# Kernel optimization log

Measured on AMD Instinct MI355X. Metric: run time of the kernel, lower is better.

The kernel has to match this reference:

```python
import jax, jax.numpy as jnp
import numpy as np

KS = 3      # kernel_size
PAD = 1     # zero padding
N = KS * KS # sampling points per pixel
PI = 3.1415926


def conv2d(x, w, b=None, stride=1, padding=0):
    out = jax.lax.conv_general_dilated(
        x, w, (stride, stride), [(padding, padding), (padding, padding)],
        dimension_numbers=('NCHW', 'OIHW', 'NCHW'))
    if b is not None:
        out = out + b[None, :, None, None]
    return out


def setup_inputs() -> dict:
    key = jax.random.key(0)
    ks = jax.random.split(key, 8)
    B, C, OUTC, H, W = 4, 64, 64, 128, 128
    x = jax.random.normal(ks[0], (B, C, H, W), jnp.float32)
    w_b = jax.random.normal(ks[1], (OUTC, C, 3, 3), jnp.float32) * 0.05
    b_b = jax.random.normal(ks[2], (OUTC,), jnp.float32) * 0.05
    w_p = jax.random.normal(ks[3], (3, C, 3, 3), jnp.float32) * 0.05
    b_p = jax.random.normal(ks[4], (3,), jnp.float32) * 0.05
    w_m = jax.random.normal(ks[5], (N, C, 3, 3), jnp.float32) * 0.05
    b_m = jax.random.normal(ks[6], (N,), jnp.float32) * 0.05
    w_c = jax.random.normal(ks[7], (OUTC, C, 3, 3), jnp.float32) * 0.05
    return {"x": x, "w_b": w_b, "b_b": b_b, "w_p": w_p, "b_p": b_p,
            "w_m": w_m, "b_m": b_m, "w_c": w_c}


def reference(x, w_b, b_b, w_p, b_p, w_m, b_m, w_c):
    B, C, H, W = x.shape
    # bias branch: plain 3x3 conv, stride 1, pad 1
    bias = conv2d(x, w_b, b_b, stride=1, padding=1)
    # offset branch: conv -> sin -> (dropout eval = id) -> sigmoid
    off = jax.nn.sigmoid(jnp.sin(conv2d(x, w_p, b_p, stride=1, padding=1)))  # [B,3,H,W]
    l = off[:, 0] * 48.5 + 1.5          # [B,H,W] rect length
    wd = off[:, 1] * 48.5 + 1.5         # [B,H,W] rect width
    theta = off[:, 2] * PI              # [B,H,W] rotation angle
    # modulation mask
    m = jax.nn.sigmoid(conv2d(x, w_m, b_m, stride=1, padding=1))  # [B,9,H,W]

    # zero-pad input for sampling
    xp = jnp.pad(x, ((0, 0), (0, 0), (PAD, PAD), (PAD, PAD)))
    Hp, Wp = H + 2 * PAD, W + 2 * PAD

    # kernel grid offsets (ij meshgrid, x flattened first)
    rng = jnp.arange(-(KS - 1) // 2, (KS - 1) // 2 + 1, dtype=jnp.float32)
    pn_x = jnp.repeat(rng, KS)  # [N]  (-1,-1,-1,0,0,0,1,1,1)
    pn_y = jnp.tile(rng, KS)    # [N]  (-1,0,1,-1,0,1,-1,0,1)
    p0_x = jnp.arange(1, H + 1, dtype=jnp.float32)[:, None, None]  # [H,1,1]
    p0_y = jnp.arange(1, W + 1, dtype=jnp.float32)[None, :, None]  # [1,W,1]

    # sampling positions p = p0 + offset/3 * p_n, per point: [B,H,W,N]
    px = p0_x + (l[..., None] / 3.0) * pn_x
    py = p0_y + (wd[..., None] / 3.0) * pn_y
    ct = jnp.cos(theta)[..., None]  # [B,H,W,1]
    st = jnp.sin(theta)[..., None]
    pxx = px * ct - py * st
    pyy = px * st + py * ct

    # integer corners (non-diff, matches .detach().floor())
    fx = jnp.floor(jax.lax.stop_gradient(pxx))
    fy = jnp.floor(jax.lax.stop_gradient(pyy))
    qlt_x = jnp.clip(fx, 0, Hp - 1).astype(jnp.int32)
    qlt_y = jnp.clip(fy, 0, Wp - 1).astype(jnp.int32)
    qrb_x = jnp.clip(fx + 1, 0, Hp - 1).astype(jnp.int32)
    qrb_y = jnp.clip(fy + 1, 0, Wp - 1).astype(jnp.int32)

    # clamp continuous positions
    pcx = jnp.clip(pxx, 0, Hp - 1)
    pcy = jnp.clip(pyy, 0, Wp - 1)

    # bilinear weights
    g_lt = (1 + (qlt_x - pcx)) * (1 + (qlt_y - pcy))
    g_rb = (1 - (qrb_x - pcx)) * (1 - (qrb_y - pcy))
    g_lb = (1 + (qlt_x - pcx)) * (1 - (qrb_y - pcy))
    g_rt = (1 - (qrb_x - pcx)) * (1 + (qlt_y - pcy))

    # gather four corners: [B,C,H,W,N]
    def _gather_one(xp_b, qx_b, qy_b):
        return xp_b[:, qx_b, qy_b]  # [C,H,W,N]
    gather = jax.vmap(_gather_one)
    x_lt = gather(xp, qlt_x, qlt_y)
    x_rb = gather(xp, qrb_x, qrb_y)
    x_lb = gather(xp, qlt_x, qrb_y)
    x_rt = gather(xp, qrb_x, qlt_y)

    x_off = (g_lt[:, None] * x_lt + g_rb[:, None] * x_rb +
             g_lb[:, None] * x_lb + g_rt[:, None] * x_rt)  # [B,C,H,W,N]
    # modulation: [B,9,H,W] -> [B,1,H,W,9]
    x_off = x_off * jnp.transpose(m, (0, 2, 3, 1))[:, None]

    # rearrange [B,C,H,W,ks*ks] -> [B,C,H*ks,W*ks]
    x_off = x_off.reshape(B, C, H, W, KS, KS)
    x_off = jnp.transpose(x_off, (0, 1, 2, 4, 3, 5)).reshape(B, C, H * KS, W * KS)

    out = conv2d(x_off, w_c, None, stride=KS, padding=0) + bias
    return out
```

## Files before the change

kernel.cpp:

```cpp
#include <hip/hip_runtime.h>
#include <hip/hip_bf16.h>
#include <math.h>

#define BB 4
#define CC 64
#define OC 64
#define HH 128
#define WW 128
#define HP 130
#define WP 130
#define KTOT 1152
#define NKK 36
#define NKC 18
#define PIXT 32

#define XP_OFF 0
#define WR8_OFF 4326400
#define WPM8_OFF (4326400 + 36864)

typedef __attribute__((ext_vector_type(8))) short bf16x8;
typedef __attribute__((ext_vector_type(4))) short bf16x4;
typedef __attribute__((ext_vector_type(4))) float f32x4;

__device__ __forceinline__ unsigned short f2bf(float v) {
    union { float f; unsigned int u; } x; x.f = v;
    unsigned int r = x.u + 0x7FFF + ((x.u >> 16) & 1);
    return (unsigned short)(r >> 16);
}

__device__ __forceinline__ unsigned short f2bfh(float v) {
    __hip_bfloat16 h = __float2bfloat16(v);
    return *reinterpret_cast<unsigned short*>(&h);
}

__device__ __forceinline__ float fexp_(float x) {
    return __builtin_amdgcn_exp2f(x * 1.44269504089f);
}
__device__ __forceinline__ float fsig_(float z) {
    return __builtin_amdgcn_rcpf(1.f + fexp_(-z));
}
__device__ __forceinline__ float fsin_(float x) {
    float r = x * 0.15915494309f;
    r = __builtin_amdgcn_fractf(r);
    return __builtin_amdgcn_sinf(r);
}
__device__ __forceinline__ float fcos_(float x) {
    float r = x * 0.15915494309f;
    r = __builtin_amdgcn_fractf(r);
    return __builtin_amdgcn_cosf(r);
}

#define NB_TR 1024
#define NB_BZ 516
#define NB_WR 288
#define NB_WPM 36

__global__ __launch_bounds__(256) void k_prep(
    const float* __restrict__ x,
    const float* __restrict__ w_b, const float* __restrict__ w_c,
    const float* __restrict__ w_p, const float* __restrict__ w_m,
    float* __restrict__ xp, unsigned short* __restrict__ wr8,
    unsigned short* __restrict__ wpm8)
{
    int bi = blockIdx.x;
    int tid = threadIdx.x;
    if (bi < NB_TR) {
        __shared__ float t[64][65];
        int b = bi >> 8;
        int h = (bi >> 1) & 127;
        int w0 = (bi & 1) * 64;
        int lane6 = tid & 63;
        for (int cc = tid >> 6; cc < 64; cc += 4)
            t[cc][lane6] = x[((b * 64 + cc) * 128 + h) * 128 + w0 + lane6];
        __syncthreads();
        for (int wsub = tid >> 6; wsub < 64; wsub += 4)
            xp[((size_t)(b * HP + h + 1) * WP + (w0 + wsub + 1)) * 64 + lane6] = t[lane6][wsub];
        return;
    }
    bi -= NB_TR;
    if (bi < NB_BZ) {
        int idx = bi * 256 + tid;
        int c = idx & 63;
        int tt = idx >> 6;
        int b = tt / 516;
        int j = tt % 516;
        int hp, wp;
        if (j < 130)      { hp = 0;       wp = j; }
        else if (j < 260) { hp = 129;     wp = j - 130; }
        else if (j < 388) { hp = j - 259; wp = 0; }
        else              { hp = j - 387; wp = 129; }
        xp[((size_t)(b * HP + hp) * WP + wp) * 64 + c] = 0.f;
        return;
    }
    bi -= NB_BZ;
    if (bi < NB_WR) {
        int idx = bi * 256 + tid;
        int j    = idx & 7;
        int lane = (idx >> 3) & 63;
        int ot   = (idx >> 9) & 3;
        int kk   = idx >> 11;
        int o  = ot * 16 + (lane & 15);
        int k  = kk * 32 + (lane >> 4) * 8 + j;
        int slot = k >> 6;
        int c    = k & 63;
        float v;
        if (slot < 9) v = w_b[((o * CC + c) * 3 + slot / 3) * 3 + slot % 3];
        else { int n = slot - 9; v = w_c[((o * CC + c) * 3 + n / 3) * 3 + n % 3]; }
        wr8[idx] = f2bf(v);
        return;
    }
    bi -= NB_WR;
    {
        int idx = bi * 256 + tid;
        if (idx >= NKC * 64 * 8) return;
        int j    = idx & 7;
        int lane = (idx >> 3) & 63;
        int kk   = idx >> 9;
        int ch = lane & 15;
        int k  = kk * 32 + (lane >> 4) * 8 + j;
        int tap = k >> 6;
        int c   = k & 63;
        float v = 0.f;
        if (ch < 3)       v = w_p[((ch * CC + c) * 3 + tap / 3) * 3 + tap % 3];
        else if (ch < 12) v = w_m[(((ch - 3) * CC + c) * 3 + tap / 3) * 3 + tap % 3];
        wpm8[idx] = f2bf(v);
    }
}

__global__ __launch_bounds__(512, 4) void k_main(
    const float* __restrict__ xp, const unsigned short* __restrict__ wr8,
    const unsigned short* __restrict__ wpm8,
    const float* __restrict__ w_p,
    const float* __restrict__ b_p, const float* __restrict__ b_m,
    const float* __restrict__ b_b, float* __restrict__ out)
{
    __shared__ unsigned short U8[2 * 18432];
    __shared__ float wth[16][9][4];

    int tid = threadIdx.x;
    int lane = tid & 63;
    int g = tid >> 6;
    int p_sub = lane >> 4;
    int cq = lane & 15;
    int c0 = cq * 4;

    int bid = blockIdx.x;
    int swz = (bid & 7) * 256 + (bid >> 3);
    int pixBase = swz * PIXT;

    for (int i = tid; i < 576; i += 512) {
        int cqi = i / 36;
        int rest = i % 36;
        int tap = rest >> 2;
        int e = rest & 3;
        int c = cqi * 4 + e;
        wth[cqi][tap][e] = w_p[((2 * CC + c) * 3 + tap / 3) * 3 + tap % 3];
    }
    __syncthreads();

    int p_local = g * 4 + p_sub;
    int ph = p_local >> 4;
    int p16 = p_local & 15;
    int pix = pixBase + p_local;
    int b = pix >> 14;
    int h = (pix >> 7) & 127;
    int w = pix & 127;
    const float* xb = xp + (size_t)b * HP * WP * 64;

    float th = 0.f;
#pragma unroll
    for (int tap = 0; tap < 9; ++tap) {
        int ti = tap / 3, tj = tap % 3;
        float4 xv = *(const float4*)&xb[((h + ti) * WP + (w + tj)) * 64 + c0];
        float4 wt = *(const float4*)&wth[cq][tap][0];
        th += xv.x * wt.x + xv.y * wt.y + xv.z * wt.z + xv.w * wt.w;
        int k = tap * 64 + c0;
        int kqt = k >> 3;
        int blk = kqt * 16 + (p16 ^ (kqt & 15));
        bf16x4 pk;
        pk[0] = (short)f2bfh(xv.x); pk[1] = (short)f2bfh(xv.y);
        pk[2] = (short)f2bfh(xv.z); pk[3] = (short)f2bfh(xv.w);
        *(bf16x4*)&U8[ph * 18432 + blk * 8 + (k & 7)] = pk;
    }
    th += __shfl_xor(th, 1);
    th += __shfl_xor(th, 2);
    th += __shfl_xor(th, 4);
    th += __shfl_xor(th, 8);

    int kq = lane >> 4;
    f32x4 ca = {0.f, 0.f, 0.f, 0.f}, cb = {0.f, 0.f, 0.f, 0.f};
    {
        int colp = lane & 3;
        int pabs = g * 4 + colp;
        int phc = g >> 2;
        int p16c = pabs & 15;
        const bf16x8* av = (const bf16x8*)wpm8;
#pragma unroll
        for (int kk = 0; kk < NKC; ++kk) {
            bf16x8 a = av[kk * 64 + lane];
            int kqt = kk * 4 + kq;
            int blk = kqt * 16 + (p16c ^ (kqt & 15));
            bf16x8 bf = *(const bf16x8*)&U8[phc * 18432 + blk * 8];
            if (kk & 1) cb = __builtin_amdgcn_mfma_f32_16x16x32_bf16(a, bf, cb, 0, 0, 0);
            else        ca = __builtin_amdgcn_mfma_f32_16x16x32_bf16(a, bf, ca, 0, 0, 0);
        }
        ca[0] += cb[0]; ca[1] += cb[1]; ca[2] += cb[2]; ca[3] += cb[3];
    }

    int base16 = p_sub << 4;
    int chc = (cq < 9) ? (3 + cq) : 3;
    int srcL = ((chc >> 2) << 4) + p_sub;
    float m0 = __shfl(ca[0], srcL);
    float m1 = __shfl(ca[1], srcL);
    float m2 = __shfl(ca[2], srcL);
    float m3 = __shfl(ca[3], srcL);
    int jj = chc & 3;
    float cm = (jj == 0) ? m0 : (jj == 1) ? m1 : (jj == 2) ? m2 : m3;
    float c0v = __shfl(ca[0], p_sub);
    float c1v = __shfl(ca[1], p_sub);

    float bp0 = b_p[0], bp1 = b_p[1], bp2 = b_p[2];
    float hval = 0.f;
    if (cq == 9)       hval = fsig_(fsin_(c0v + bp0)) * 48.5f + 1.5f;
    else if (cq == 10) hval = fsig_(fsin_(c1v + bp1)) * 48.5f + 1.5f;
    else if (cq == 11) hval = fcos_(fsig_(fsin_(th + bp2)) * 3.1415926f);
    else if (cq == 12) hval = fsin_(fsig_(fsin_(th + bp2)) * 3.1415926f);
    float l  = __shfl(hval, base16 + 9);
    float wd = __shfl(hval, base16 + 10);
    float ct = __shfl(hval, base16 + 11);
    float st = __shfl(hval, base16 + 12);

    unsigned int qpack; float glt, grb, glb, grt;
    {
        int n = (cq < 9) ? cq : 8;
        float mm = fsig_(cm + b_m[n]);
        float pnx = (float)(n / 3 - 1);
        float pny = (float)(n % 3 - 1);
        float px = (float)(h + 1) + (l * (1.f / 3.f)) * pnx;
        float py = (float)(w + 1) + (wd * (1.f / 3.f)) * pny;
        float pxx = px * ct - py * st;
        float pyy = px * st + py * ct;
        float fx = floorf(pxx);
        float fy = floorf(pyy);
        int qltx = min(max((int)fx, 0), HP - 1);
        int qlty = min(max((int)fy, 0), WP - 1);
        int qrbx = min(max((int)fx + 1, 0), HP - 1);
        int qrby = min(max((int)fy + 1, 0), WP - 1);
        float pcx = fminf(fmaxf(pxx, 0.f), (float)(HP - 1));
        float pcy = fminf(fmaxf(pyy, 0.f), (float)(WP - 1));
        float dltx = 1.f + ((float)qltx - pcx);
        float drbx = 1.f - ((float)qrbx - pcx);
        float dlty = 1.f + ((float)qlty - pcy);
        float drby = 1.f - ((float)qrby - pcy);
        glt = dltx * dlty * mm;
        grb = drbx * drby * mm;
        glb = dltx * drby * mm;
        grt = drbx * dlty * mm;
        qpack = (unsigned)qltx | ((unsigned)qlty << 8) |
                ((unsigned)qrbx << 16) | ((unsigned)qrby << 24);
    }

    unsigned int qn[9];
    float wlt[9], wrb[9], wlb[9], wrt[9];
#pragma unroll
    for (int n = 0; n < 9; ++n) {
        qn[n]  = __shfl(qpack, base16 + n);
        wlt[n] = __shfl(glt, base16 + n);
        wrb[n] = __shfl(grb, base16 + n);
        wlb[n] = __shfl(glb, base16 + n);
        wrt[n] = __shfl(grt, base16 + n);
    }

#pragma unroll
    for (int n = 0; n < 9; ++n) {
        unsigned int q = qn[n];
        int qltx = q & 255, qlty = (q >> 8) & 255;
        int qrbx = (q >> 16) & 255, qrby = (q >> 24) & 255;
        float4 xlt = *(const float4*)&xb[(qltx * WP + qlty) * 64 + c0];
        float4 xrb = *(const float4*)&xb[(qrbx * WP + qrby) * 64 + c0];
        float4 xlb = *(const float4*)&xb[(qltx * WP + qrby) * 64 + c0];
        float4 xrt = *(const float4*)&xb[(qrbx * WP + qlty) * 64 + c0];
        float g_lt = wlt[n], g_rb = wrb[n], g_lb = wlb[n], g_rt = wrt[n];
        float v0 = g_lt * xlt.x + g_rb * xrb.x + g_lb * xlb.x + g_rt * xrt.x;
        float v1 = g_lt * xlt.y + g_rb * xrb.y + g_lb * xlb.y + g_rt * xrt.y;
        float v2 = g_lt * xlt.z + g_rb * xrb.z + g_lb * xlb.z + g_rt * xrt.z;
        float v3 = g_lt * xlt.w + g_rb * xrb.w + g_lb * xlb.w + g_rt * xrt.w;
        int k = (9 + n) * 64 + c0;
        int kqt = k >> 3;
        int blk = kqt * 16 + (p16 ^ (kqt & 15));
        bf16x4 pk;
        pk[0] = (short)f2bfh(v0); pk[1] = (short)f2bfh(v1);
        pk[2] = (short)f2bfh(v2); pk[3] = (short)f2bfh(v3);
        *(bf16x4*)&U8[ph * 18432 + blk * 8 + (k & 7)] = pk;
    }
    __syncthreads();

    int ot = g & 3;
    int ph2 = g >> 2;
    int pn = lane & 15;
    f32x4 a0 = {0.f, 0.f, 0.f, 0.f}, a1 = {0.f, 0.f, 0.f, 0.f};
    const bf16x8* wv = (const bf16x8*)wr8;
#pragma unroll
    for (int kk = 0; kk < NKK; ++kk) {
        bf16x8 a = wv[(kk * 4 + ot) * 64 + lane];
        int kqt = kk * 4 + kq;
        int blk = kqt * 16 + (pn ^ (kqt & 15));
        bf16x8 bf = *(const bf16x8*)&U8[ph2 * 18432 + blk * 8];
        if (kk & 1) a1 = __builtin_amdgcn_mfma_f32_16x16x32_bf16(a, bf, a1, 0, 0, 0);
        else        a0 = __builtin_amdgcn_mfma_f32_16x16x32_bf16(a, bf, a0, 0, 0, 0);
    }

    int pix2 = pixBase + ph2 * 16 + pn;
    int bb2 = pix2 >> 14;
    int hw = pix2 & 16383;
#pragma unroll
    for (int r2 = 0; r2 < 4; ++r2) {
        int o = ot * 16 + kq * 4 + r2;
        out[((size_t)(bb2 * 64 + o)) * 16384 + hw] = a0[r2] + a1[r2] + b_b[o];
    }
}

extern "C" void kernel_launch(void* const* d_in, const int* in_sizes, int n_in,
                              void* d_out, int out_size, void* d_ws, size_t ws_size,
                              hipStream_t stream) {
    const float* x   = (const float*)d_in[0];
    const float* w_b = (const float*)d_in[1];
    const float* b_b = (const float*)d_in[2];
    const float* w_p = (const float*)d_in[3];
    const float* b_p = (const float*)d_in[4];
    const float* w_m = (const float*)d_in[5];
    const float* b_m = (const float*)d_in[6];
    const float* w_c = (const float*)d_in[7];
    float* out = (float*)d_out;

    float* ws = (float*)d_ws;
    float* xp = ws + XP_OFF;
    unsigned short* wr8  = (unsigned short*)(ws + WR8_OFF);
    unsigned short* wpm8 = (unsigned short*)(ws + WPM8_OFF);

    k_prep<<<NB_TR + NB_BZ + NB_WR + NB_WPM, 256, 0, stream>>>(
        x, w_b, w_c, w_p, w_m, xp, wr8, wpm8);
    k_main<<<(BB * HH * WW) / PIXT, 512, 0, stream>>>(
        xp, wr8, wpm8, w_p, b_p, b_m, b_b, out);
}
```

Before: 70.13 us.

## Double pixel tile per block to reuse weight fragments across two MFMA tiles

Each block now processes 64 pixels instead of 32. It runs the sampling and packing stage twice into a doubled LDS buffer, then in the main GEMM loads each weight fragment once and feeds two MFMAs, one per 16-pixel half. This halves global weight-fragment traffic per pixel and halves the block count. The cost is twice the LDS per block (about 147KB), lower occupancy (launch bounds 2), and serialized gather work per block.

```diff
diff --git a/kernel.cpp b/kernel.cpp
--- a/kernel.cpp
+++ b/kernel.cpp
@@ -12,7 +12,7 @@
 #define KTOT 1152
 #define NKK 36
 #define NKC 18
-#define PIXT 32
+#define PIXT 64
 
 #define XP_OFF 0
 #define WR8_OFF 4326400
@@ -127,14 +127,14 @@
     }
 }
 
-__global__ __launch_bounds__(512, 4) void k_main(
+__global__ __launch_bounds__(512, 2) void k_main(
     const float* __restrict__ xp, const unsigned short* __restrict__ wr8,
     const unsigned short* __restrict__ wpm8,
     const float* __restrict__ w_p,
     const float* __restrict__ b_p, const float* __restrict__ b_m,
     const float* __restrict__ b_b, float* __restrict__ out)
 {
-    __shared__ unsigned short U8[2 * 18432];
+    __shared__ unsigned short U8[4 * 18432];
     __shared__ float wth[16][9][4];
 
     int tid = threadIdx.x;
@@ -143,9 +143,10 @@
     int p_sub = lane >> 4;
     int cq = lane & 15;
     int c0 = cq * 4;
+    int kq = lane >> 4;
 
     int bid = blockIdx.x;
-    int swz = (bid & 7) * 256 + (bid >> 3);
+    int swz = (bid & 7) * 128 + (bid >> 3);
     int pixBase = swz * PIXT;
 
     for (int i = tid; i < 576; i += 512) {
@@ -158,165 +159,179 @@
     }
     __syncthreads();
 
-    int p_local = g * 4 + p_sub;
-    int ph = p_local >> 4;
-    int p16 = p_local & 15;
-    int pix = pixBase + p_local;
-    int b = pix >> 14;
-    int h = (pix >> 7) & 127;
-    int w = pix & 127;
-    const float* xb = xp + (size_t)b * HP * WP * 64;
-
-    float th = 0.f;
-#pragma unroll
-    for (int tap = 0; tap < 9; ++tap) {
-        int ti = tap / 3, tj = tap % 3;
-        float4 xv = *(const float4*)&xb[((h + ti) * WP + (w + tj)) * 64 + c0];
-        float4 wt = *(const float4*)&wth[cq][tap][0];
-        th += xv.x * wt.x + xv.y * wt.y + xv.z * wt.z + xv.w * wt.w;
-        int k = tap * 64 + c0;
-        int kqt = k >> 3;
-        int blk = kqt * 16 + (p16 ^ (kqt & 15));
-        bf16x4 pk;
-        pk[0] = (short)f2bfh(xv.x); pk[1] = (short)f2bfh(xv.y);
-        pk[2] = (short)f2bfh(xv.z); pk[3] = (short)f2bfh(xv.w);
-        *(bf16x4*)&U8[ph * 18432 + blk * 8 + (k & 7)] = pk;
-    }
-    th += __shfl_xor(th, 1);
-    th += __shfl_xor(th, 2);
-    th += __shfl_xor(th, 4);
-    th += __shfl_xor(th, 8);
-
-    int kq = lane >> 4;
-    f32x4 ca = {0.f, 0.f, 0.f, 0.f}, cb = {0.f, 0.f, 0.f, 0.f};
-    {
-        int colp = lane & 3;
-        int pabs = g * 4 + colp;
-        int phc = g >> 2;
-        int p16c = pabs & 15;
-        const bf16x8* av = (const bf16x8*)wpm8;
-#pragma unroll
-        for (int kk = 0; kk < NKC; ++kk) {
-            bf16x8 a = av[kk * 64 + lane];
-            int kqt = kk * 4 + kq;
-            int blk = kqt * 16 + (p16c ^ (kqt & 15));
-            bf16x8 bf = *(const bf16x8*)&U8[phc * 18432 + blk * 8];
-            if (kk & 1) cb = __builtin_amdgcn_mfma_f32_16x16x32_bf16(a, bf, cb, 0, 0, 0);
-            else        ca = __builtin_amdgcn_mfma_f32_16x16x32_bf16(a, bf, ca, 0, 0, 0);
-        }
-        ca[0] += cb[0]; ca[1] += cb[1]; ca[2] += cb[2]; ca[3] += cb[3];
-    }
-
-    int base16 = p_sub << 4;
-    int chc = (cq < 9) ? (3 + cq) : 3;
-    int srcL = ((chc >> 2) << 4) + p_sub;
-    float m0 = __shfl(ca[0], srcL);
-    float m1 = __shfl(ca[1], srcL);
-    float m2 = __shfl(ca[2], srcL);
-    float m3 = __shfl(ca[3], srcL);
-    int jj = chc & 3;
-    float cm = (jj == 0) ? m0 : (jj == 1) ? m1 : (jj == 2) ? m2 : m3;
-    float c0v = __shfl(ca[0], p_sub);
-    float c1v = __shfl(ca[1], p_sub);
-
-    float bp0 = b_p[0], bp1 = b_p[1], bp2 = b_p[2];
-    float hval = 0.f;
-    if (cq == 9)       hval = fsig_(fsin_(c0v + bp0)) * 48.5f + 1.5f;
-    else if (cq == 10) hval = fsig_(fsin_(c1v + bp1)) * 48.5f + 1.5f;
-    else if (cq == 11) hval = fcos_(fsig_(fsin_(th + bp2)) * 3.1415926f);
-    else if (cq == 12) hval = fsin_(fsig_(fsin_(th + bp2)) * 3.1415926f);
-    float l  = __shfl(hval, base16 + 9);
-    float wd = __shfl(hval, base16 + 10);
-    float ct = __shfl(hval, base16 + 11);
-    float st = __shfl(hval, base16 + 12);
-
-    unsigned int qpack; float glt, grb, glb, grt;
-    {
-        int n = (cq < 9) ? cq : 8;
-        float mm = fsig_(cm + b_m[n]);
-        float pnx = (float)(n / 3 - 1);
-        float pny = (float)(n % 3 - 1);
-        float px = (float)(h + 1) + (l * (1.f / 3.f)) * pnx;
-        float py = (float)(w + 1) + (wd * (1.f / 3.f)) * pny;
-        float pxx = px * ct - py * st;
-        float pyy = px * st + py * ct;
-        float fx = floorf(pxx);
-        float fy = floorf(pyy);
-        int qltx = min(max((int)fx, 0), HP - 1);
-        int qlty = min(max((int)fy, 0), WP - 1);
-        int qrbx = min(max((int)fx + 1, 0), HP - 1);
-        int qrby = min(max((int)fy + 1, 0), WP - 1);
-        float pcx = fminf(fmaxf(pxx, 0.f), (float)(HP - 1));
-        float pcy = fminf(fmaxf(pyy, 0.f), (float)(WP - 1));
-        float dltx = 1.f + ((float)qltx - pcx);
-        float drbx = 1.f - ((float)qrbx - pcx);
-        float dlty = 1.f + ((float)qlty - pcy);
-        float drby = 1.f - ((float)qrby - pcy);
-        glt = dltx * dlty * mm;
-        grb = drbx * drby * mm;
-        glb = dltx * drby * mm;
-        grt = drbx * dlty * mm;
-        qpack = (unsigned)qltx | ((unsigned)qlty << 8) |
-                ((unsigned)qrbx << 16) | ((unsigned)qrby << 24);
-    }
-
-    unsigned int qn[9];
-    float wlt[9], wrb[9], wlb[9], wrt[9];
-#pragma unroll
-    for (int n = 0; n < 9; ++n) {
-        qn[n]  = __shfl(qpack, base16 + n);
-        wlt[n] = __shfl(glt, base16 + n);
-        wrb[n] = __shfl(grb, base16 + n);
-        wlb[n] = __shfl(glb, base16 + n);
-        wrt[n] = __shfl(grt, base16 + n);
-    }
-
-#pragma unroll
-    for (int n = 0; n < 9; ++n) {
-        unsigned int q = qn[n];
-        int qltx = q & 255, qlty = (q >> 8) & 255;
-        int qrbx = (q >> 16) & 255, qrby = (q >> 24) & 255;
-        float4 xlt = *(const float4*)&xb[(qltx * WP + qlty) * 64 + c0];
-        float4 xrb = *(const float4*)&xb[(qrbx * WP + qrby) * 64 + c0];
-        float4 xlb = *(const float4*)&xb[(qltx * WP + qrby) * 64 + c0];
-        float4 xrt = *(const float4*)&xb[(qrbx * WP + qlty) * 64 + c0];
-        float g_lt = wlt[n], g_rb = wrb[n], g_lb = wlb[n], g_rt = wrt[n];
-        float v0 = g_lt * xlt.x + g_rb * xrb.x + g_lb * xlb.x + g_rt * xrt.x;
-        float v1 = g_lt * xlt.y + g_rb * xrb.y + g_lb * xlb.y + g_rt * xrt.y;
-        float v2 = g_lt * xlt.z + g_rb * xrb.z + g_lb * xlb.z + g_rt * xrt.z;
-        float v3 = g_lt * xlt.w + g_rb * xrb.w + g_lb * xlb.w + g_rt * xrt.w;
-        int k = (9 + n) * 64 + c0;
-        int kqt = k >> 3;
-        int blk = kqt * 16 + (p16 ^ (kqt & 15));
-        bf16x4 pk;
-        pk[0] = (short)f2bfh(v0); pk[1] = (short)f2bfh(v1);
-        pk[2] = (short)f2bfh(v2); pk[3] = (short)f2bfh(v3);
-        *(bf16x4*)&U8[ph * 18432 + blk * 8 + (k & 7)] = pk;
+    for (int pp = 0; pp < 2; ++pp) {
+        int p_local = g * 4 + p_sub + pp * 32;
+        int ph = p_local >> 4;
+        int p16 = p_local & 15;
+        int pix = pixBase + p_local;
+        int b = pix >> 14;
+        int h = (pix >> 7) & 127;
+        int w = pix & 127;
+        const float* xb = xp + (size_t)b * HP * WP * 64;
+
+        float th = 0.f;
+#pragma unroll
+        for (int tap = 0; tap < 9; ++tap) {
+            int ti = tap / 3, tj = tap % 3;
+            float4 xv = *(const float4*)&xb[((h + ti) * WP + (w + tj)) * 64 + c0];
+            float4 wt = *(const float4*)&wth[cq][tap][0];
+            th += xv.x * wt.x + xv.y * wt.y + xv.z * wt.z + xv.w * wt.w;
+            int k = tap * 64 + c0;
+            int kqt = k >> 3;
+            int blk = kqt * 16 + (p16 ^ (kqt & 15));
+            bf16x4 pk;
+            pk[0] = (short)f2bfh(xv.x); pk[1] = (short)f2bfh(xv.y);
+            pk[2] = (short)f2bfh(xv.z); pk[3] = (short)f2bfh(xv.w);
+            *(bf16x4*)&U8[ph * 18432 + blk * 8 + (k & 7)] = pk;
+        }
+        th += __shfl_xor(th, 1);
+        th += __shfl_xor(th, 2);
+        th += __shfl_xor(th, 4);
+        th += __shfl_xor(th, 8);
+
+        f32x4 ca = {0.f, 0.f, 0.f, 0.f}, cb = {0.f, 0.f, 0.f, 0.f};
+        {
+            int colp = lane & 3;
+            int pabs = g * 4 + colp;
+            int phc = (g >> 2) + 2 * pp;
+            int p16c = pabs & 15;
+            const bf16x8* av = (const bf16x8*)wpm8;
+#pragma unroll
+            for (int kk = 0; kk < NKC; ++kk) {
+                bf16x8 a = av[kk * 64 + lane];
+                int kqt = kk * 4 + kq;
+                int blk = kqt * 16 + (p16c ^ (kqt & 15));
+                bf16x8 bf = *(const bf16x8*)&U8[phc * 18432 + blk * 8];
+                if (kk & 1) cb = __builtin_amdgcn_mfma_f32_16x16x32_bf16(a, bf, cb, 0, 0, 0);
+                else        ca = __builtin_amdgcn_mfma_f32_16x16x32_bf16(a, bf, ca, 0, 0, 0);
+            }
+            ca[0] += cb[0]; ca[1] += cb[1]; ca[2] += cb[2]; ca[3] += cb[3];
+        }
+
+        int base16 = p_sub << 4;
+        int chc = (cq < 9) ? (3 + cq) : 3;
+        int srcL = ((chc >> 2) << 4) + p_sub;
+        float m0 = __shfl(ca[0], srcL);
+        float m1 = __shfl(ca[1], srcL);
+        float m2 = __shfl(ca[2], srcL);
+        float m3 = __shfl(ca[3], srcL);
+        int jj = chc & 3;
+        float cm = (jj == 0) ? m0 : (jj == 1) ? m1 : (jj == 2) ? m2 : m3;
+        float c0v = __shfl(ca[0], p_sub);
+        float c1v = __shfl(ca[1], p_sub);
+
+        float bp0 = b_p[0], bp1 = b_p[1], bp2 = b_p[2];
+        float hval = 0.f;
+        if (cq == 9)       hval = fsig_(fsin_(c0v + bp0)) * 48.5f + 1.5f;
+        else if (cq == 10) hval = fsig_(fsin_(c1v + bp1)) * 48.5f + 1.5f;
+        else if (cq == 11) hval = fcos_(fsig_(fsin_(th + bp2)) * 3.1415926f);
+        else if (cq == 12) hval = fsin_(fsig_(fsin_(th + bp2)) * 3.1415926f);
+        float l  = __shfl(hval, base16 + 9);
+        float wd = __shfl(hval, base16 + 10);
+        float ct = __shfl(hval, base16 + 11);
+        float st = __shfl(hval, base16 + 12);
+
+        unsigned int qpack; float glt, grb, glb, grt;
+        {
+            int n = (cq < 9) ? cq : 8;
+            float mm = fsig_(cm + b_m[n]);
+            float pnx = (float)(n / 3 - 1);
+            float pny = (float)(n % 3 - 1);
+            float px = (float)(h + 1) + (l * (1.f / 3.f)) * pnx;
+            float py = (float)(w + 1) + (wd * (1.f / 3.f)) * pny;
+            float pxx = px * ct - py * st;
+            float pyy = px * st + py * ct;
+            float fx = floorf(pxx);
+            float fy = floorf(pyy);
+            int qltx = min(max((int)fx, 0), HP - 1);
+            int qlty = min(max((int)fy, 0), WP - 1);
+            int qrbx = min(max((int)fx + 1, 0), HP - 1);
+            int qrby = min(max((int)fy + 1, 0), WP - 1);
+            float pcx = fminf(fmaxf(pxx, 0.f), (float)(HP - 1));
+            float pcy = fminf(fmaxf(pyy, 0.f), (float)(WP - 1));
+            float dltx = 1.f + ((float)qltx - pcx);
+            float drbx = 1.f - ((float)qrbx - pcx);
+            float dlty = 1.f + ((float)qlty - pcy);
+            float drby = 1.f - ((float)qrby - pcy);
+            glt = dltx * dlty * mm;
+            grb = drbx * drby * mm;
+            glb = dltx * drby * mm;
+            grt = drbx * dlty * mm;
+            qpack = (unsigned)qltx | ((unsigned)qlty << 8) |
+                    ((unsigned)qrbx << 16) | ((unsigned)qrby << 24);
+        }
+
+        unsigned int qn[9];
+        float wlt[9], wrb[9], wlb[9], wrt[9];
+#pragma unroll
+        for (int n = 0; n < 9; ++n) {
+            qn[n]  = __shfl(qpack, base16 + n);
+            wlt[n] = __shfl(glt, base16 + n);
+            wrb[n] = __shfl(grb, base16 + n);
+            wlb[n] = __shfl(glb, base16 + n);
+            wrt[n] = __shfl(grt, base16 + n);
+        }
+
+#pragma unroll
+        for (int n = 0; n < 9; ++n) {
+            unsigned int q = qn[n];
+            int qltx = q & 255, qlty = (q >> 8) & 255;
+            int qrbx = (q >> 16) & 255, qrby = (q >> 24) & 255;
+            float4 xlt = *(const float4*)&xb[(qltx * WP + qlty) * 64 + c0];
+            float4 xrb = *(const float4*)&xb[(qrbx * WP + qrby) * 64 + c0];
+            float4 xlb = *(const float4*)&xb[(qltx * WP + qrby) * 64 + c0];
+            float4 xrt = *(const float4*)&xb[(qrbx * WP + qlty) * 64 + c0];
+            float g_lt = wlt[n], g_rb = wrb[n], g_lb = wlb[n], g_rt = wrt[n];
+            float v0 = g_lt * xlt.x + g_rb * xrb.x + g_lb * xlb.x + g_rt * xrt.x;
+            float v1 = g_lt * xlt.y + g_rb * xrb.y + g_lb * xlb.y + g_rt * xrt.y;
+            float v2 = g_lt * xlt.z + g_rb * xrb.z + g_lb * xlb.z + g_rt * xrt.z;
+            float v3 = g_lt * xlt.w + g_rb * xrb.w + g_lb * xlb.w + g_rt * xrt.w;
+            int k = (9 + n) * 64 + c0;
+            int kqt = k >> 3;
+            int blk = kqt * 16 + (p16 ^ (kqt & 15));
+            bf16x4 pk;
+            pk[0] = (short)f2bfh(v0); pk[1] = (short)f2bfh(v1);
+            pk[2] = (short)f2bfh(v2); pk[3] = (short)f2bfh(v3);
+            *(bf16x4*)&U8[ph * 18432 + blk * 8 + (k & 7)] = pk;
+        }
     }
     __syncthreads();
 
     int ot = g & 3;
-    int ph2 = g >> 2;
+    int hA = g >> 2;
     int pn = lane & 15;
-    f32x4 a0 = {0.f, 0.f, 0.f, 0.f}, a1 = {0.f, 0.f, 0.f, 0.f};
+    f32x4 accA = {0.f, 0.f, 0.f, 0.f}, accB = {0.f, 0.f, 0.f, 0.f};
     const bf16x8* wv = (const bf16x8*)wr8;
 #pragma unroll
     for (int kk = 0; kk < NKK; ++kk) {
         bf16x8 a = wv[(kk * 4 + ot) * 64 + lane];
         int kqt = kk * 4 + kq;
         int blk = kqt * 16 + (pn ^ (kqt & 15));
-        bf16x8 bf = *(const bf16x8*)&U8[ph2 * 18432 + blk * 8];
-        if (kk & 1) a1 = __builtin_amdgcn_mfma_f32_16x16x32_bf16(a, bf, a1, 0, 0, 0);
-        else        a0 = __builtin_amdgcn_mfma_f32_16x16x32_bf16(a, bf, a0, 0, 0, 0);
-    }
-
-    int pix2 = pixBase + ph2 * 16 + pn;
-    int bb2 = pix2 >> 14;
-    int hw = pix2 & 16383;
-#pragma unroll
-    for (int r2 = 0; r2 < 4; ++r2) {
-        int o = ot * 16 + kq * 4 + r2;
-        out[((size_t)(bb2 * 64 + o)) * 16384 + hw] = a0[r2] + a1[r2] + b_b[o];
+        bf16x8 bA = *(const bf16x8*)&U8[hA * 18432 + blk * 8];
+        bf16x8 bB = *(const bf16x8*)&U8[(hA + 2) * 18432 + blk * 8];
+        accA = __builtin_amdgcn_mfma_f32_16x16x32_bf16(a, bA, accA, 0, 0, 0);
+        accB = __builtin_amdgcn_mfma_f32_16x16x32_bf16(a, bB, accB, 0, 0, 0);
+    }
+
+    {
+        int pix2 = pixBase + hA * 16 + pn;
+        int bb2 = pix2 >> 14;
+        int hw = pix2 & 16383;
+#pragma unroll
+        for (int r2 = 0; r2 < 4; ++r2) {
+            int o = ot * 16 + kq * 4 + r2;
+            out[((size_t)(bb2 * 64 + o)) * 16384 + hw] = accA[r2] + b_b[o];
+        }
+    }
+    {
+        int pix2 = pixBase + (hA + 2) * 16 + pn;
+        int bb2 = pix2 >> 14;
+        int hw = pix2 & 16383;
+#pragma unroll
+        for (int r2 = 0; r2 < 4; ++r2) {
+            int o = ot * 16 + kq * 4 + r2;
+            out[((size_t)(bb2 * 64 + o)) * 16384 + hw] = accB[r2] + b_b[o];
+        }
     }
 }
 
```

After: 79.03 us. +12.7%, slower.

## Halve LDS staging by splitting main GEMM into two K-phases, stage sampling records in LDS

Applied to the files above, without the earlier changes.

The kernel used to stage the whole K=1152 B operand (plain taps plus deformed taps) in LDS before one GEMM. It now stages only the plain taps and runs the first half of the GEMM, then overwrites the same buffer with the bilinear-sampled deformed values and runs the second half. Per-tap sampling indices and weights move from register shuffles into a small LDS record array, which frees registers. Launch bounds rise from 4 to 6 blocks, aiming for higher occupancy at the cost of extra barriers.

```diff
diff --git a/kernel.cpp b/kernel.cpp
--- a/kernel.cpp
+++ b/kernel.cpp
@@ -127,14 +127,15 @@
     }
 }
 
-__global__ __launch_bounds__(512, 4) void k_main(
+__global__ __launch_bounds__(512, 6) void k_main(
     const float* __restrict__ xp, const unsigned short* __restrict__ wr8,
     const unsigned short* __restrict__ wpm8,
     const float* __restrict__ w_p,
     const float* __restrict__ b_p, const float* __restrict__ b_m,
     const float* __restrict__ b_b, float* __restrict__ out)
 {
-    __shared__ unsigned short U8[2 * 18432];
+    __shared__ unsigned short U8[2 * 9216];
+    __shared__ unsigned int rec[32][9][5];
     __shared__ float wth[16][9][4];
 
     int tid = threadIdx.x;
@@ -143,6 +144,7 @@
     int p_sub = lane >> 4;
     int cq = lane & 15;
     int c0 = cq * 4;
+    int kq = lane >> 4;
 
     int bid = blockIdx.x;
     int swz = (bid & 7) * 256 + (bid >> 3);
@@ -180,14 +182,13 @@
         bf16x4 pk;
         pk[0] = (short)f2bfh(xv.x); pk[1] = (short)f2bfh(xv.y);
         pk[2] = (short)f2bfh(xv.z); pk[3] = (short)f2bfh(xv.w);
-        *(bf16x4*)&U8[ph * 18432 + blk * 8 + (k & 7)] = pk;
+        *(bf16x4*)&U8[ph * 9216 + blk * 8 + (k & 7)] = pk;
     }
     th += __shfl_xor(th, 1);
     th += __shfl_xor(th, 2);
     th += __shfl_xor(th, 4);
     th += __shfl_xor(th, 8);
 
-    int kq = lane >> 4;
     f32x4 ca = {0.f, 0.f, 0.f, 0.f}, cb = {0.f, 0.f, 0.f, 0.f};
     {
         int colp = lane & 3;
@@ -200,7 +201,7 @@
             bf16x8 a = av[kk * 64 + lane];
             int kqt = kk * 4 + kq;
             int blk = kqt * 16 + (p16c ^ (kqt & 15));
-            bf16x8 bf = *(const bf16x8*)&U8[phc * 18432 + blk * 8];
+            bf16x8 bf = *(const bf16x8*)&U8[phc * 9216 + blk * 8];
             if (kk & 1) cb = __builtin_amdgcn_mfma_f32_16x16x32_bf16(a, bf, cb, 0, 0, 0);
             else        ca = __builtin_amdgcn_mfma_f32_16x16x32_bf16(a, bf, ca, 0, 0, 0);
         }
@@ -230,7 +231,6 @@
     float ct = __shfl(hval, base16 + 11);
     float st = __shfl(hval, base16 + 12);
 
-    unsigned int qpack; float glt, grb, glb, grt;
     {
         int n = (cq < 9) ? cq : 8;
         float mm = fsig_(cm + b_m[n]);
@@ -252,60 +252,74 @@
         float drbx = 1.f - ((float)qrbx - pcx);
         float dlty = 1.f + ((float)qlty - pcy);
         float drby = 1.f - ((float)qrby - pcy);
-        glt = dltx * dlty * mm;
-        grb = drbx * drby * mm;
-        glb = dltx * drby * mm;
-        grt = drbx * dlty * mm;
-        qpack = (unsigned)qltx | ((unsigned)qlty << 8) |
-                ((unsigned)qrbx << 16) | ((unsigned)qrby << 24);
-    }
-
-    unsigned int qn[9];
-    float wlt[9], wrb[9], wlb[9], wrt[9];
+        float glt = dltx * dlty * mm;
+        float grb = drbx * drby * mm;
+        float glb = dltx * drby * mm;
+        float grt = drbx * dlty * mm;
+        unsigned int qpack = (unsigned)qltx | ((unsigned)qlty << 8) |
+                             ((unsigned)qrbx << 16) | ((unsigned)qrby << 24);
+        if (cq < 9) {
+            unsigned int* r = &rec[p_local][cq][0];
+            r[0] = qpack;
+            r[1] = __float_as_uint(glt);
+            r[2] = __float_as_uint(grb);
+            r[3] = __float_as_uint(glb);
+            r[4] = __float_as_uint(grt);
+        }
+    }
+    __syncthreads();
+
+    int ot = g & 3;
+    int ph2 = g >> 2;
+    int pn = lane & 15;
+    f32x4 a0 = {0.f, 0.f, 0.f, 0.f}, a1 = {0.f, 0.f, 0.f, 0.f};
+    const bf16x8* wv = (const bf16x8*)wr8;
+#pragma unroll
+    for (int kk = 0; kk < 18; ++kk) {
+        bf16x8 a = wv[(kk * 4 + ot) * 64 + lane];
+        int kqt = kk * 4 + kq;
+        int blk = kqt * 16 + (pn ^ (kqt & 15));
+        bf16x8 bf = *(const bf16x8*)&U8[ph2 * 9216 + blk * 8];
+        if (kk & 1) a1 = __builtin_amdgcn_mfma_f32_16x16x32_bf16(a, bf, a1, 0, 0, 0);
+        else        a0 = __builtin_amdgcn_mfma_f32_16x16x32_bf16(a, bf, a0, 0, 0, 0);
+    }
+    __syncthreads();
+
 #pragma unroll
     for (int n = 0; n < 9; ++n) {
-        qn[n]  = __shfl(qpack, base16 + n);
-        wlt[n] = __shfl(glt, base16 + n);
-        wrb[n] = __shfl(grb, base16 + n);
-        wlb[n] = __shfl(glb, base16 + n);
-        wrt[n] = __shfl(grt, base16 + n);
-    }
-
-#pragma unroll
-    for (int n = 0; n < 9; ++n) {
-        unsigned int q = qn[n];
+        const unsigned int* r = &rec[p_local][n][0];
+        unsigned int q = r[0];
+        float g_lt = __uint_as_float(r[1]);
+        float g_rb = __uint_as_float(r[2]);
+        float g_lb = __uint_as_float(r[3]);
+        float g_rt = __uint_as_float(r[4]);
         int qltx = q & 255, qlty = (q >> 8) & 255;
         int qrbx = (q >> 16) & 255, qrby = (q >> 24) & 255;
         float4 xlt = *(const float4*)&xb[(qltx * WP + qlty) * 64 + c0];
         float4 xrb = *(const float4*)&xb[(qrbx * WP + qrby) * 64 + c0];
         float4 xlb = *(const float4*)&xb[(qltx * WP + qrby) * 64 + c0];
         float4 xrt = *(const float4*)&xb[(qrbx * WP + qlty) * 64 + c0];
-        float g_lt = wlt[n], g_rb = wrb[n], g_lb = wlb[n], g_rt = wrt[n];
         float v0 = g_lt * xlt.x + g_rb * xrb.x + g_lb * xlb.x + g_rt * xrt.x;
         float v1 = g_lt * xlt.y + g_rb * xrb.y + g_lb * xlb.y + g_rt * xrt.y;
         float v2 = g_lt * xlt.z + g_rb * xrb.z + g_lb * xlb.z + g_rt * xrt.z;
         float v3 = g_lt * xlt.w + g_rb * xrb.w + g_lb * xlb.w + g_rt * xrt.w;
-        int k = (9 + n) * 64 + c0;
+        int k = n * 64 + c0;
         int kqt = k >> 3;
         int blk = kqt * 16 + (p16 ^ (kqt & 15));
         bf16x4 pk;
         pk[0] = (short)f2bfh(v0); pk[1] = (short)f2bfh(v1);
         pk[2] = (short)f2bfh(v2); pk[3] = (short)f2bfh(v3);
-        *(bf16x4*)&U8[ph * 18432 + blk * 8 + (k & 7)] = pk;
+        *(bf16x4*)&U8[ph * 9216 + blk * 8 + (k & 7)] = pk;
     }
     __syncthreads();
 
-    int ot = g & 3;
-    int ph2 = g >> 2;
-    int pn = lane & 15;
-    f32x4 a0 = {0.f, 0.f, 0.f, 0.f}, a1 = {0.f, 0.f, 0.f, 0.f};
-    const bf16x8* wv = (const bf16x8*)wr8;
-#pragma unroll
-    for (int kk = 0; kk < NKK; ++kk) {
+#pragma unroll
+    for (int kk = 18; kk < 36; ++kk) {
         bf16x8 a = wv[(kk * 4 + ot) * 64 + lane];
-        int kqt = kk * 4 + kq;
+        int kl = kk - 18;
+        int kqt = kl * 4 + kq;
         int blk = kqt * 16 + (pn ^ (kqt & 15));
-        bf16x8 bf = *(const bf16x8*)&U8[ph2 * 18432 + blk * 8];
+        bf16x8 bf = *(const bf16x8*)&U8[ph2 * 9216 + blk * 8];
         if (kk & 1) a1 = __builtin_amdgcn_mfma_f32_16x16x32_bf16(a, bf, a1, 0, 0, 0);
         else        a0 = __builtin_amdgcn_mfma_f32_16x16x32_bf16(a, bf, a0, 0, 0, 0);
     }
```

Result: slower. 74.82 us (+6.7%).
